# Kernel optimization log

Hardware: AMD Instinct MI355X
Metric: run time of the kernel (lower is better)

The kernel has to match this reference:

```python
import jax, jax.numpy as jnp
import numpy as np
import math

B, S, E, H = 4, 2048, 1024, 16
D = E // H  # head_dim = 64


def setup_inputs() -> dict:
    key = jax.random.key(0)
    ks = jax.random.split(key, 5)
    scale = 1.0 / math.sqrt(E)
    x = jax.random.normal(ks[0], (B, S, E), dtype=jnp.float32)
    attention_mask = jnp.ones((B, S), dtype=jnp.int32)
    W_qkv = jax.random.normal(ks[1], (E, 3 * E), dtype=jnp.float32) * scale
    b_qkv = jnp.zeros((3 * E,), dtype=jnp.float32)
    W_proj = jax.random.normal(ks[2], (E, E), dtype=jnp.float32) * scale
    b_proj = jnp.zeros((E,), dtype=jnp.float32)
    return {"x": x, "attention_mask": attention_mask, "W_qkv": W_qkv,
            "b_qkv": b_qkv, "W_proj": W_proj, "b_proj": b_proj}


def reference(x, attention_mask, W_qkv, b_qkv, W_proj, b_proj):
    b, s, e = x.shape
    qkv = x @ W_qkv + b_qkv                       # [B,S,3E]
    qkv = qkv.reshape(b, s, 3, H, D)
    qkv = jnp.transpose(qkv, (2, 0, 3, 1, 4))     # [3,B,H,S,D]
    q, k, v = qkv[0], qkv[1], qkv[2]
    scores = jnp.einsum('bhqd,bhkd->bhqk', q, k) / math.sqrt(D)
    causal = jnp.tril(jnp.ones((s, s), dtype=bool))[None, None]  # [1,1,S,S]
    neg_inf = jnp.float32(-jnp.inf)
    scores = jnp.where(causal, scores, neg_inf)
    pad = (attention_mask[:, None, None, :s] != 0)               # [B,1,1,S]
    scores = jnp.where(pad, scores, neg_inf)
    attn = jax.nn.softmax(scores, axis=-1)        # dropout=0.0 (eval mode)
    out = jnp.einsum('bhqk,bhkd->bhqd', attn, v)  # [B,H,S,D]
    out = jnp.transpose(out, (0, 2, 1, 3)).reshape(b, s, e)
    return out @ W_proj + b_proj
```

## Files before the change

kernel.cpp:

```cpp
#include <hip/hip_runtime.h>
#include <hip/hip_bf16.h>
#include <cstdint>
#include <cstddef>

#define B_ 4
#define S_ 2048
#define E_ 1024
#define H_ 16
#define D_ 64
#define NEG_BIG (-1e30f)
#define SC2 0.18033688011112043f

typedef __bf16 bf16x8 __attribute__((ext_vector_type(8)));
typedef __bf16 bf16x4v __attribute__((ext_vector_type(4)));
typedef float f32x4 __attribute__((ext_vector_type(4)));
typedef float f32x16 __attribute__((ext_vector_type(16)));

__device__ __forceinline__ void async_copy16(void* lds, const void* g) {
  __builtin_amdgcn_global_load_lds(
      (const __attribute__((address_space(1))) void*)g,
      (__attribute__((address_space(3))) void*)lds, 16, 0, 0);
}

__device__ __forceinline__ float bfu2f(unsigned short u) {
  unsigned v = ((unsigned)u) << 16;
  float f;
  __builtin_memcpy(&f, &v, 4);
  return f;
}
__device__ __forceinline__ unsigned short f2bfu(float f) {
  __hip_bfloat16 h = __float2bfloat16(f);
  unsigned short u;
  __builtin_memcpy(&u, &h, 2);
  return u;
}
__device__ __forceinline__ unsigned pk2(float a, float b) {
  return (unsigned)f2bfu(a) | ((unsigned)f2bfu(b) << 16);
}

__device__ __forceinline__ void pl32swap(unsigned& a, unsigned& b) {
#if defined(__has_builtin)
#if __has_builtin(__builtin_amdgcn_permlane32_swap)
  typedef int i32x2 __attribute__((ext_vector_type(2)));
  i32x2 r = __builtin_amdgcn_permlane32_swap((int)a, (int)b, false, false);
  a = (unsigned)r[0];
  b = (unsigned)r[1];
  return;
#else
  asm("v_permlane32_swap_b32 %0, %1" : "+v"(a), "+v"(b));
  return;
#endif
#else
  asm("v_permlane32_swap_b32 %0, %1" : "+v"(a), "+v"(b));
#endif
}

__global__ __launch_bounds__(256) void probe_dtype(
    const unsigned short* __restrict__ xr, int* __restrict__ flagp) {
  __shared__ int cnt;
  if (threadIdx.x == 0) cnt = 0;
  __syncthreads();
  int bad = 0;
  for (int i = 0; i < 32; ++i) {
    unsigned short u = xr[(threadIdx.x * 32 + i) * 2];
    int e = (u >> 7) & 0xFF;
    if (e == 0xFF || e >= 0x90 || (e != 0 && e <= 0x60)) bad++;
  }
  atomicAdd(&cnt, bad);
  __syncthreads();
  if (threadIdx.x == 0) {
    flagp[0] = (cnt > 512) ? 0 : 1;
    flagp[1] = 1;
  }
}

__global__ __launch_bounds__(256) void prep(
    const int* __restrict__ am, float* __restrict__ mb,
    int* __restrict__ flagp,
    const void* __restrict__ bq_in, float* __restrict__ bq,
    const void* __restrict__ bp_in, float* __restrict__ bp) {
  int i = blockIdx.x * 256 + threadIdx.x;
  const int flag = flagp[0];
  if (i < 8192) {
    int a = am[i];
    mb[i] = a ? 0.f : NEG_BIG;
    if (a == 0) atomicAnd(flagp + 1, 0);
  } else if (i < 11264) {
    int j = i - 8192;
    bq[j] = (flag == 0) ? ((const float*)bq_in)[j]
                        : bfu2f(((const unsigned short*)bq_in)[j]);
  } else if (i < 12288) {
    int j = i - 11264;
    bp[j] = (flag == 0) ? ((const float*)bp_in)[j]
                        : bfu2f(((const unsigned short*)bp_in)[j]);
  }
}

__global__ __launch_bounds__(256) void conv_x_bf16(
    const void* __restrict__ in, long long off,
    unsigned short* __restrict__ out,
    const int* __restrict__ flagp, int n8) {
  int i = blockIdx.x * 256 + threadIdx.x;
  if (i >= n8) return;
  if (*flagp == 0) {
    const float* p = (const float*)in + off + (size_t)i * 8;
    float4 a = *(const float4*)p;
    float4 b = *(const float4*)(p + 4);
    uint4 o = make_uint4(pk2(a.x, a.y), pk2(a.z, a.w), pk2(b.x, b.y), pk2(b.z, b.w));
    *(uint4*)(out + (size_t)i * 8) = o;
  } else {
    const unsigned short* p = (const unsigned short*)in + off + (size_t)i * 8;
    *(uint4*)(out + (size_t)i * 8) = *(const uint4*)p;
  }
}

__global__ __launch_bounds__(256) void transpose_conv(
    const void* __restrict__ in, unsigned short* __restrict__ out,
    const int* __restrict__ flagp, int R, int C) {
  __shared__ unsigned short t[32][33];
  const int flag = *flagp;
  const int c0 = blockIdx.x * 32, r0 = blockIdx.y * 32;
  const int lc = threadIdx.x & 31, lr = threadIdx.x >> 5;
  for (int i = 0; i < 4; ++i) {
    int r = lr + i * 8;
    size_t idx = (size_t)(r0 + r) * C + c0 + lc;
    t[r][lc] = (flag == 0) ? f2bfu(((const float*)in)[idx])
                           : ((const unsigned short*)in)[idx];
  }
  __syncthreads();
  for (int i = 0; i < 4; ++i) {
    int r = lr + i * 8;
    out[(size_t)(c0 + r) * R + r0 + lc] = t[lc][r];
  }
}

__global__ __launch_bounds__(256) void gemm_bb(
    const __hip_bfloat16* __restrict__ A,
    const __hip_bfloat16* __restrict__ Bt,
    const float* __restrict__ bias,
    const int* __restrict__ flagp, int outmode,
    void* __restrict__ Cv, long long coff,
    int M, int N, int K) {
  __shared__ __align__(16) __hip_bfloat16 SH[2][128 * 64];
  __hip_bfloat16* As = SH[0];
  __hip_bfloat16* Bs = SH[1];
  const int flag = *flagp;
  const int tid = threadIdx.x;
  const int lin = blockIdx.x;
  const int mtiles = M >> 7;
  const int mloc = mtiles >> 3;
  const int msh = 31 - __builtin_clz(mloc);
  const int xcd = lin & 7, idx = lin >> 3;
  const int m0 = (xcd * mloc + (idx & (mloc - 1))) << 7;
  const int n0 = (idx >> msh) << 7;
  const int w = tid >> 6, lane = tid & 63;
  const int wm = (w & 1) * 64, wn = (w >> 1) * 64;
  const int lm = lane & 15, kg = lane >> 4;

  f32x4 acc[4][4] = {};

  for (int k0 = 0; k0 < K; k0 += 64) {
    __syncthreads();
    #pragma unroll
    for (int c = 0; c < 4; ++c) {
      int o = tid * 16 + c * 4096;
      int row = o >> 7, chp = (o >> 4) & 7;
      int gch = chp ^ (row & 7);
      async_copy16((char*)As + o, (const char*)(A + (size_t)(m0 + row) * K + k0 + gch * 8));
      async_copy16((char*)Bs + o, (const char*)(Bt + (size_t)(n0 + row) * K + k0 + gch * 8));
    }
    __syncthreads();
    #pragma unroll
    for (int kk = 0; kk < 2; ++kk) {
      bf16x8 af[4], bff[4];
      #pragma unroll
      for (int t = 0; t < 4; ++t) {
        int rt = wm + t * 16 + lm;
        int ch = (kk * 4 + kg) ^ (rt & 7);
        af[t] = *(const bf16x8*)(As + rt * 64 + ch * 8);
        int rb = wn + t * 16 + lm;
        int chb = (kk * 4 + kg) ^ (rb & 7);
        bff[t] = *(const bf16x8*)(Bs + rb * 64 + chb * 8);
      }
      #pragma unroll
      for (int tm = 0; tm < 4; ++tm)
        #pragma unroll
        for (int tn = 0; tn < 4; ++tn)
          acc[tm][tn] = __builtin_amdgcn_mfma_f32_16x16x32_bf16(af[tm], bff[tn], acc[tm][tn], 0, 0, 0);
    }
  }

  const bool f32out = (outmode != 0 && flag == 0);
  if (f32out) {
    for (int tn = 0; tn < 4; ++tn) {
      int col = n0 + wn + tn * 16 + lm;
      float bv = bias[col];
      for (int tm = 0; tm < 4; ++tm) {
        int rbase = m0 + wm + tm * 16 + kg * 4;
        for (int r = 0; r < 4; ++r)
          ((float*)Cv)[(size_t)coff + (size_t)(rbase + r) * N + col] =
              acc[tm][tn][r] + bv;
      }
    }
  } else {
    for (int hp = 0; hp < 2; ++hp) {
      __syncthreads();
      if (wm == hp * 64) {
        __hip_bfloat16* Cs16 = (__hip_bfloat16*)SH;
        #pragma unroll
        for (int tn = 0; tn < 4; ++tn) {
          int col = wn + tn * 16 + lm;
          float bv = bias[n0 + col];
          #pragma unroll
          for (int tm = 0; tm < 4; ++tm)
            #pragma unroll
            for (int r = 0; r < 4; ++r)
              Cs16[(tm * 16 + kg * 4 + r) * 136 + col] =
                  __float2bfloat16(acc[tm][tn][r] + bv);
        }
      }
      __syncthreads();
      const __hip_bfloat16* Cs16 = (const __hip_bfloat16*)SH;
      unsigned short* outp = (unsigned short*)Cv + coff;
      #pragma unroll
      for (int rd = 0; rd < 4; ++rd) {
        int chunk = rd * 256 + tid;
        int row = chunk >> 4, cch = chunk & 15;
        uint4 v = *(const uint4*)(Cs16 + row * 136 + cch * 8);
        *(uint4*)(outp + (size_t)(m0 + hp * 64 + row) * N + n0 + cch * 8) = v;
      }
    }
  }
}

#define VSTR 72
__device__ __forceinline__ void attn_subtile(
    int j0s, int wq_min, int wq_max, int qg, int allones,
    const char* kbyte, const float* mbrow,
    uint4& kc0, uint4& kc1, uint4& kc2, uint4& kc3,
    uint4& kn0, uint4& kn1, uint4& kn2, uint4& kn3,
    const bf16x8* bq, const __hip_bfloat16* VTb, int hi,
    float& mrow, float& plocal, f32x16& o0, f32x16& o1) {
  if (j0s > wq_max) return;
  {
    const int jn = j0s + 32;
    if (jn <= wq_max) {
      const char* kp = kbyte + (size_t)jn * 6144;
      kn0 = *(const uint4*)(kp);
      kn1 = *(const uint4*)(kp + 32);
      kn2 = *(const uint4*)(kp + 64);
      kn3 = *(const uint4*)(kp + 96);
    }
  }
  bf16x8 a0, a1, a2, a3;
  __builtin_memcpy(&a0, &kc0, 16);
  __builtin_memcpy(&a1, &kc1, 16);
  __builtin_memcpy(&a2, &kc2, 16);
  __builtin_memcpy(&a3, &kc3, 16);

  f32x16 sacc = {};
  __builtin_amdgcn_s_setprio(1);
  sacc = __builtin_amdgcn_mfma_f32_32x32x16_bf16(a0, bq[0], sacc, 0, 0, 0);
  sacc = __builtin_amdgcn_mfma_f32_32x32x16_bf16(a1, bq[1], sacc, 0, 0, 0);
  sacc = __builtin_amdgcn_mfma_f32_32x32x16_bf16(a2, bq[2], sacc, 0, 0, 0);
  sacc = __builtin_amdgcn_mfma_f32_32x32x16_bf16(a3, bq[3], sacc, 0, 0, 0);
  __builtin_amdgcn_s_setprio(0);

  float mt = NEG_BIG;
  const bool needc = (j0s + 31 > wq_min);
  if (allones) {
    if (needc) {
      #pragma unroll
      for (int r = 0; r < 16; ++r) {
        int key = j0s + (r & 3) + 8 * (r >> 2) + 4 * hi;
        float v = (key <= qg) ? sacc[r] : NEG_BIG;
        sacc[r] = v;
        mt = fmaxf(mt, v);
      }
    } else {
      #pragma unroll
      for (int r = 0; r < 16; ++r) mt = fmaxf(mt, sacc[r]);
    }
    mt *= SC2;
  } else {
    #pragma unroll
    for (int rr = 0; rr < 4; ++rr) {
      float4 mb4 = *(const float4*)(mbrow + j0s + rr * 8 + hi * 4);
      const float* mp = (const float*)&mb4;
      #pragma unroll
      for (int i = 0; i < 4; ++i) {
        int r = rr * 4 + i;
        int key = j0s + i + 8 * rr + 4 * hi;
        float v = fmaf(sacc[r], SC2, mp[i]);
        if (needc) v = (key <= qg) ? v : NEG_BIG;
        sacc[r] = v;
        mt = fmaxf(mt, v);
      }
    }
  }
  mt = fmaxf(mt, __shfl_xor(mt, 32));

  if (!__all(mt <= mrow + 8.f)) {
    float mn = fmaxf(mrow, mt);
    float a = __builtin_exp2f(mrow - mn);
    plocal *= a;
    #pragma unroll
    for (int r = 0; r < 16; ++r) { o0[r] *= a; o1[r] *= a; }
    mrow = mn;
  }

  const float sfac = allones ? SC2 : 1.0f;
  float psl = 0.f;
  unsigned pk[8];
  #pragma unroll
  for (int r2 = 0; r2 < 8; ++r2) {
    float p0 = __builtin_exp2f(fmaf(sacc[2 * r2],     sfac, -mrow));
    float p1 = __builtin_exp2f(fmaf(sacc[2 * r2 + 1], sfac, -mrow));
    psl += p0 + p1;
    pk[r2] = pk2(p0, p1);
  }
  plocal += psl;

  pl32swap(pk[0], pk[2]);
  pl32swap(pk[1], pk[3]);
  pl32swap(pk[4], pk[6]);
  pl32swap(pk[5], pk[7]);

  __builtin_amdgcn_s_setprio(1);
  #pragma unroll
  for (int ks = 0; ks < 2; ++ks) {
    uint4 t = make_uint4(pk[ks * 4 + 0], pk[ks * 4 + 1],
                         pk[ks * 4 + 2], pk[ks * 4 + 3]);
    bf16x8 bp;
    __builtin_memcpy(&bp, &t, 16);
    bf16x8 av0 = *(const bf16x8*)(VTb + ks * 16);
    bf16x8 av1 = *(const bf16x8*)(VTb + 32 * VSTR + ks * 16);
    o0 = __builtin_amdgcn_mfma_f32_32x32x16_bf16(av0, bp, o0, 0, 0, 0);
    o1 = __builtin_amdgcn_mfma_f32_32x32x16_bf16(av1, bp, o1, 0, 0, 0);
  }
  __builtin_amdgcn_s_setprio(0);
}

__global__ __launch_bounds__(256, 3) void attn_flash(
    const __hip_bfloat16* __restrict__ qkv,
    const float* __restrict__ mbias,
    const int* __restrict__ flags,
    __hip_bfloat16* __restrict__ outp) {
  __shared__ __align__(16) __hip_bfloat16 VT[2][64 * VSTR];

  const int tid = threadIdx.x;
  const int lin = blockIdx.x;
  const int nbh = gridDim.x >> 4;
  const int bhloc = nbh >> 3;
  const int bsh = 31 - __builtin_clz(bhloc);
  const int xcd = lin & 7, idx = lin >> 3;
  const int bh = xcd * bhloc + (idx & (bhloc - 1));
  const int bx = idx >> bsh;
  const int qt = 15 - bx;
  const int b = bh >> 4, h = bh & 15;
  const int q0 = qt * 128;
  const size_t rowbase = (size_t)b * S_;
  const int w = tid >> 6, lane = tid & 63;
  const int l31 = lane & 31, hi = lane >> 5;
  const int qg = q0 + w * 32 + l31;
  const int wq_min = q0 + w * 32, wq_max = wq_min + 31;
  const int allones = flags[1];
  const float* mbrow = mbias + rowbase;

  const char* kbyte = (const char*)(qkv + (rowbase + l31) * 3072 + 1024 + h * 64 + hi * 8);

  bf16x8 bq[4];
  {
    const __hip_bfloat16* qp = qkv + (rowbase + qg) * 3072 + h * 64 + hi * 8;
    bq[0] = *(const bf16x8*)(qp);
    bq[1] = *(const bf16x8*)(qp + 16);
    bq[2] = *(const bf16x8*)(qp + 32);
    bq[3] = *(const bf16x8*)(qp + 48);
  }

  const int jmax = 2 * qt + 1;

  uint4 ka0, ka1, ka2, ka3, kb0, kb1, kb2, kb3;
  ka0 = *(const uint4*)(kbyte);
  ka1 = *(const uint4*)(kbyte + 32);
  ka2 = *(const uint4*)(kbyte + 64);
  ka3 = *(const uint4*)(kbyte + 96);
  {
    const __hip_bfloat16* vp = qkv + (rowbase + lane) * 3072 + 2048 + h * 64 + w * 16;
    uint4 v0 = *(const uint4*)(vp);
    uint4 v1 = *(const uint4*)(vp + 8);
    const __hip_bfloat16* p0 = (const __hip_bfloat16*)&v0;
    const __hip_bfloat16* p1 = (const __hip_bfloat16*)&v1;
    #pragma unroll
    for (int e = 0; e < 8; ++e) {
      VT[0][(w * 16 + e) * VSTR + lane] = p0[e];
      VT[0][(w * 16 + 8 + e) * VSTR + lane] = p1[e];
    }
  }

  float mrow = NEG_BIG, plocal = 0.f;
  f32x16 o0 = {}, o1 = {};
  int buf = 0;

  for (int j = 0; j <= jmax; ++j) {
    __syncthreads();
    const int nbuf = buf ^ 1;
    const int j0 = j * 64;
    const bool pre = (j < jmax);
    uint4 vva, vvb;
    if (pre) {
      const __hip_bfloat16* vp = qkv + (rowbase + j0 + 64 + lane) * 3072 + 2048 + h * 64 + w * 16;
      vva = *(const uint4*)(vp);
      vvb = *(const uint4*)(vp + 8);
    }
    const __hip_bfloat16* vb0 = VT[buf] + l31 * VSTR + hi * 8;

    attn_subtile(j0, wq_min, wq_max, qg, allones, kbyte, mbrow,
                 ka0, ka1, ka2, ka3, kb0, kb1, kb2, kb3,
                 bq, vb0, hi, mrow, plocal, o0, o1);
    attn_subtile(j0 + 32, wq_min, wq_max, qg, allones, kbyte, mbrow,
                 kb0, kb1, kb2, kb3, ka0, ka1, ka2, ka3,
                 bq, vb0 + 32, hi, mrow, plocal, o0, o1);

    if (pre) {
      const __hip_bfloat16* p0 = (const __hip_bfloat16*)&vva;
      const __hip_bfloat16* p1 = (const __hip_bfloat16*)&vvb;
      #pragma unroll
      for (int e = 0; e < 8; ++e) {
        VT[nbuf][(w * 16 + e) * VSTR + lane] = p0[e];
        VT[nbuf][(w * 16 + 8 + e) * VSTR + lane] = p1[e];
      }
    }
    buf = nbuf;
  }

  {
    float l = plocal + __shfl_xor(plocal, 32);
    float linv = (l > 0.f) ? 1.f / l : 0.f;
    __hip_bfloat16* ob = outp + (rowbase + qg) * 1024 + h * 64;
    #pragma unroll
    for (int rr = 0; rr < 4; ++rr) {
      bf16x4v ov;
      ov[0] = (__bf16)(o0[rr * 4 + 0] * linv);
      ov[1] = (__bf16)(o0[rr * 4 + 1] * linv);
      ov[2] = (__bf16)(o0[rr * 4 + 2] * linv);
      ov[3] = (__bf16)(o0[rr * 4 + 3] * linv);
      *(bf16x4v*)(ob + rr * 8 + hi * 4) = ov;
      bf16x4v ow;
      ow[0] = (__bf16)(o1[rr * 4 + 0] * linv);
      ow[1] = (__bf16)(o1[rr * 4 + 1] * linv);
      ow[2] = (__bf16)(o1[rr * 4 + 2] * linv);
      ow[3] = (__bf16)(o1[rr * 4 + 3] * linv);
      *(bf16x4v*)(ob + 32 + rr * 8 + hi * 4) = ow;
    }
  }
}

extern "C" void kernel_launch(void* const* d_in, const int* in_sizes, int n_in,
                              void* d_out, int out_size, void* d_ws, size_t ws_size,
                              hipStream_t stream) {
  const bool merged = (ws_size >= (80ull << 20));
  char* ws = (char*)d_ws;
  int*            flag   = (int*)ws;
  float*          bq     = (float*)(ws + 1024);
  float*          bp     = (float*)(ws + 16384);
  float*          mbias  = (float*)(ws + 32768);
  unsigned short* WqkvTu = (unsigned short*)(ws + 65536);
  unsigned short* WprojTu= (unsigned short*)(ws + 65536 + 6291456);
  char*           big    = ws + 65536 + 8388608;
  __hip_bfloat16* qkv    = (__hip_bfloat16*)big;
  char*           anx    = big + (merged ? 50331648u : 12582912u);
  __hip_bfloat16* attno  = (__hip_bfloat16*)anx;
  unsigned short* xbf    = (unsigned short*)anx;

  probe_dtype<<<1, 256, 0, stream>>>((const unsigned short*)d_in[0], flag);
  prep<<<48, 256, 0, stream>>>((const int*)d_in[1], mbias, flag,
                               d_in[3], bq, d_in[5], bp);
  transpose_conv<<<dim3(96, 32), 256, 0, stream>>>(d_in[2], WqkvTu, flag, 1024, 3072);
  transpose_conv<<<dim3(32, 32), 256, 0, stream>>>(d_in[4], WprojTu, flag, 1024, 1024);

  const int nchunk = merged ? 1 : B_;
  const int bsz = merged ? B_ : 1;
  const int Mc = bsz * S_;
  for (int c = 0; c < nchunk; ++c) {
    long long off = (long long)c * S_ * E_;
    conv_x_bf16<<<dim3((Mc * 1024) / 2048), 256, 0, stream>>>(
        d_in[0], off, xbf, flag, (Mc * 1024) / 8);
    gemm_bb<<<dim3((Mc / 128) * (3072 / 128)), 256, 0, stream>>>(
        (const __hip_bfloat16*)xbf, (const __hip_bfloat16*)WqkvTu, bq, flag, 0,
        qkv, 0, Mc, 3072, 1024);
    attn_flash<<<dim3((S_ / 128) * (bsz * H_)), 256, 0, stream>>>(
        qkv, mbias + (size_t)c * S_, flag, attno);
    gemm_bb<<<dim3((Mc / 128) * (1024 / 128)), 256, 0, stream>>>(
        attno, (const __hip_bfloat16*)WprojTu, bp, flag, 1,
        d_out, off, Mc, 1024, 1024);
  }
}
```

Before: 299.5 us.

## Double-buffer GEMM LDS tiles and enlarge block to 256x128 with 512 threads

```diff
diff --git a/kernel.cpp b/kernel.cpp
--- a/kernel.cpp
+++ b/kernel.cpp
@@ -134,53 +134,72 @@
   }
 }
 
-__global__ __launch_bounds__(256) void gemm_bb(
+__global__ __launch_bounds__(512, 2) void gemm_bb(
     const __hip_bfloat16* __restrict__ A,
     const __hip_bfloat16* __restrict__ Bt,
     const float* __restrict__ bias,
     const int* __restrict__ flagp, int outmode,
     void* __restrict__ Cv, long long coff,
     int M, int N, int K) {
-  __shared__ __align__(16) __hip_bfloat16 SH[2][128 * 64];
-  __hip_bfloat16* As = SH[0];
-  __hip_bfloat16* Bs = SH[1];
+  __shared__ __align__(16) char LDSC[98304];
   const int flag = *flagp;
   const int tid = threadIdx.x;
   const int lin = blockIdx.x;
-  const int mtiles = M >> 7;
+  const int mtiles = M >> 8;
   const int mloc = mtiles >> 3;
   const int msh = 31 - __builtin_clz(mloc);
   const int xcd = lin & 7, idx = lin >> 3;
-  const int m0 = (xcd * mloc + (idx & (mloc - 1))) << 7;
+  const int m0 = (xcd * mloc + (idx & (mloc - 1))) << 8;
   const int n0 = (idx >> msh) << 7;
   const int w = tid >> 6, lane = tid & 63;
-  const int wm = (w & 1) * 64, wn = (w >> 1) * 64;
+  const int wm = (w >> 1) * 64, wn = (w & 1) * 64;
   const int lm = lane & 15, kg = lane >> 4;
+  const int NT = K >> 6;
 
   f32x4 acc[4][4] = {};
 
-  for (int k0 = 0; k0 < K; k0 += 64) {
-    __syncthreads();
-    #pragma unroll
-    for (int c = 0; c < 4; ++c) {
-      int o = tid * 16 + c * 4096;
-      int row = o >> 7, chp = (o >> 4) & 7;
-      int gch = chp ^ (row & 7);
-      async_copy16((char*)As + o, (const char*)(A + (size_t)(m0 + row) * K + k0 + gch * 8));
-      async_copy16((char*)Bs + o, (const char*)(Bt + (size_t)(n0 + row) * K + k0 + gch * 8));
-    }
-    __syncthreads();
+#define STAGE_TILE(bufi, ti)                                                   \
+  do {                                                                         \
+    const int k0s = (ti) << 6;                                                 \
+    char* Ab_ = LDSC + (bufi) * 32768;                                         \
+    char* Bb_ = LDSC + 65536 + (bufi) * 16384;                                 \
+    _Pragma("unroll")                                                          \
+    for (int c = 0; c < 4; ++c) {                                              \
+      int q = c * 512 + tid;                                                   \
+      int row = q >> 3, chp = q & 7;                                           \
+      int gch = chp ^ (row & 7);                                               \
+      async_copy16(Ab_ + q * 16,                                               \
+                   (const char*)(A + (size_t)(m0 + row) * K + k0s + gch * 8)); \
+    }                                                                          \
+    _Pragma("unroll")                                                          \
+    for (int c = 0; c < 2; ++c) {                                              \
+      int q = c * 512 + tid;                                                   \
+      int row = q >> 3, chp = q & 7;                                           \
+      int gch = chp ^ (row & 7);                                               \
+      async_copy16(Bb_ + q * 16,                                               \
+                   (const char*)(Bt + (size_t)(n0 + row) * K + k0s + gch * 8));\
+    }                                                                          \
+  } while (0)
+
+  STAGE_TILE(0, 0);
+  __syncthreads();
+
+  int buf = 0;
+  for (int t = 0; t < NT; ++t) {
+    if (t + 1 < NT) STAGE_TILE(buf ^ 1, t + 1);
+    const __hip_bfloat16* Ab = (const __hip_bfloat16*)(LDSC + buf * 32768);
+    const __hip_bfloat16* Bb = (const __hip_bfloat16*)(LDSC + 65536 + buf * 16384);
     #pragma unroll
     for (int kk = 0; kk < 2; ++kk) {
       bf16x8 af[4], bff[4];
       #pragma unroll
-      for (int t = 0; t < 4; ++t) {
-        int rt = wm + t * 16 + lm;
+      for (int tt = 0; tt < 4; ++tt) {
+        int rt = wm + tt * 16 + lm;
         int ch = (kk * 4 + kg) ^ (rt & 7);
-        af[t] = *(const bf16x8*)(As + rt * 64 + ch * 8);
-        int rb = wn + t * 16 + lm;
+        af[tt] = *(const bf16x8*)(Ab + rt * 64 + ch * 8);
+        int rb = wn + tt * 16 + lm;
         int chb = (kk * 4 + kg) ^ (rb & 7);
-        bff[t] = *(const bf16x8*)(Bs + rb * 64 + chb * 8);
+        bff[tt] = *(const bf16x8*)(Bb + rb * 64 + chb * 8);
       }
       #pragma unroll
       for (int tm = 0; tm < 4; ++tm)
@@ -188,6 +207,8 @@
         for (int tn = 0; tn < 4; ++tn)
           acc[tm][tn] = __builtin_amdgcn_mfma_f32_16x16x32_bf16(af[tm], bff[tn], acc[tm][tn], 0, 0, 0);
     }
+    __syncthreads();
+    buf ^= 1;
   }
 
   const bool f32out = (outmode != 0 && flag == 0);
@@ -203,10 +224,10 @@
       }
     }
   } else {
-    for (int hp = 0; hp < 2; ++hp) {
+    for (int hp = 0; hp < 4; ++hp) {
       __syncthreads();
-      if (wm == hp * 64) {
-        __hip_bfloat16* Cs16 = (__hip_bfloat16*)SH;
+      if ((w >> 1) == hp) {
+        __hip_bfloat16* Cs16 = (__hip_bfloat16*)LDSC;
         #pragma unroll
         for (int tn = 0; tn < 4; ++tn) {
           int col = wn + tn * 16 + lm;
@@ -220,17 +241,18 @@
         }
       }
       __syncthreads();
-      const __hip_bfloat16* Cs16 = (const __hip_bfloat16*)SH;
+      const __hip_bfloat16* Cs16 = (const __hip_bfloat16*)LDSC;
       unsigned short* outp = (unsigned short*)Cv + coff;
       #pragma unroll
-      for (int rd = 0; rd < 4; ++rd) {
-        int chunk = rd * 256 + tid;
+      for (int rd = 0; rd < 2; ++rd) {
+        int chunk = rd * 512 + tid;
         int row = chunk >> 4, cch = chunk & 15;
         uint4 v = *(const uint4*)(Cs16 + row * 136 + cch * 8);
         *(uint4*)(outp + (size_t)(m0 + hp * 64 + row) * N + n0 + cch * 8) = v;
       }
     }
   }
+#undef STAGE_TILE
 }
 
 #define VSTR 72
@@ -486,12 +508,12 @@
     long long off = (long long)c * S_ * E_;
     conv_x_bf16<<<dim3((Mc * 1024) / 2048), 256, 0, stream>>>(
         d_in[0], off, xbf, flag, (Mc * 1024) / 8);
-    gemm_bb<<<dim3((Mc / 128) * (3072 / 128)), 256, 0, stream>>>(
+    gemm_bb<<<dim3((Mc / 256) * (3072 / 128)), 512, 0, stream>>>(
         (const __hip_bfloat16*)xbf, (const __hip_bfloat16*)WqkvTu, bq, flag, 0,
         qkv, 0, Mc, 3072, 1024);
     attn_flash<<<dim3((S_ / 128) * (bsz * H_)), 256, 0, stream>>>(
         qkv, mbias + (size_t)c * S_, flag, attno);
-    gemm_bb<<<dim3((Mc / 128) * (1024 / 128)), 256, 0, stream>>>(
+    gemm_bb<<<dim3((Mc / 256) * (1024 / 128)), 512, 0, stream>>>(
         attno, (const __hip_bfloat16*)WprojTu, bp, flag, 1,
         d_out, off, Mc, 1024, 1024);
   }
```

New measurement: 301.3 us. No clear change (+0.6%).
